# Kernel optimization log

Hardware: AMD Instinct MI355X
Metric: run time of the kernel (lower is better)

The kernel has to match this reference:

```python
import jax, jax.numpy as jnp
import numpy as np

B, S, Dm, H = 2, 2048, 1024, 16
HD = Dm // H            # 64, head dim == rotary dim
INTER = 4096            # intermediate_size (gated: W1 -> 2*INTER)
EPS = 1e-5


def _rotate_half(x):
    x1, x2 = jnp.split(x, 2, axis=-1)
    return jnp.concatenate((-x2, x1), axis=-1)


def _layernorm(x, g, b):
    mu = jnp.mean(x, axis=-1, keepdims=True)
    var = jnp.var(x, axis=-1, keepdims=True)
    return (x - mu) * jax.lax.rsqrt(var + EPS) * g + b


def setup_inputs() -> dict:
    key = jax.random.key(0)
    ks = jax.random.split(key, 12)
    s = 0.02
    hidden_states = jax.random.normal(ks[0], (B, S, Dm), jnp.float32)
    attention_mask = jnp.zeros((B, 1, 1, S), jnp.float32)
    # RoPE angles: pos * inv_freq, shape [S, HD]
    inv_freq = 1.0 / (10000.0 ** (jnp.arange(0, HD, 2, dtype=jnp.float32) / HD))
    ang = jnp.arange(S, dtype=jnp.float32)[:, None] * inv_freq[None, :]
    rope_freqs = jnp.concatenate([ang, ang], axis=-1)  # [S, HD]
    params = {
        'Wq': jax.random.normal(ks[1], (Dm, Dm)) * s, 'bq': jnp.zeros((Dm,)),
        'Wk': jax.random.normal(ks[2], (Dm, Dm)) * s, 'bk': jnp.zeros((Dm,)),
        'Wv': jax.random.normal(ks[3], (Dm, Dm)) * s, 'bv': jnp.zeros((Dm,)),
        'Wo': jax.random.normal(ks[4], (Dm, Dm)) * s, 'bo': jnp.zeros((Dm,)),
        'ln1_g': jnp.ones((Dm,)), 'ln1_b': jnp.zeros((Dm,)),
        'ln2_g': jnp.ones((Dm,)), 'ln2_b': jnp.zeros((Dm,)),
        'W1': jax.random.normal(ks[5], (Dm, 2 * INTER)) * s, 'b1': jnp.zeros((2 * INTER,)),
        'W2': jax.random.normal(ks[6], (INTER, Dm)) * s, 'b2': jnp.zeros((Dm,)),
    }
    return {'hidden_states': hidden_states, 'attention_mask': attention_mask,
            'rope_freqs': rope_freqs, **params}


def reference(hidden_states, attention_mask, rope_freqs,
              Wq, bq, Wk, bk, Wv, bv, Wo, bo,
              ln1_g, ln1_b, ln2_g, ln2_b, W1, b1, W2, b2):
    # ---- attention block (pre-LN) ----
    x = _layernorm(hidden_states, ln1_g, ln1_b)          # [B,S,Dm]
    def heads(t):  # [B,S,Dm] -> [B,H,S,HD]
        return t.reshape(B, S, H, HD).transpose(0, 2, 1, 3)
    q = heads(x @ Wq + bq)
    k = heads(x @ Wk + bk)
    v = heads(x @ Wv + bv)
    # RoPE (full head dim rotated)
    cos = jnp.cos(rope_freqs)[None, None, :, :]          # [1,1,S,HD]
    sin = jnp.sin(rope_freqs)[None, None, :, :]
    q = q * cos + _rotate_half(q) * sin
    k = k * cos + _rotate_half(k) * sin
    scores = jnp.einsum('bhqd,bhkd->bhqk', q, k) / jnp.sqrt(jnp.float32(HD))
    scores = scores + attention_mask
    probs = jax.nn.softmax(scores, axis=-1)
    probs = jnp.where(attention_mask < -1e-5, 0.0, probs)  # masked_fill
    ctx = jnp.einsum('bhqk,bhkd->bhqd', probs, v)
    ctx = ctx.transpose(0, 2, 1, 3).reshape(B, S, Dm)
    hidden = hidden_states + (ctx @ Wo + bo)              # residual
    # ---- MLP block (pre-LN, swiglu) ----
    y = _layernorm(hidden, ln2_g, ln2_b)
    h = y @ W1 + b1
    h0, h1 = jnp.split(h, 2, axis=-1)
    act = h0 * jax.nn.silu(h1)                            # swiglu
    out = hidden + (act @ W2 + b2)
    return out
```

## Files before the change

kernel.cpp:

```cpp
#include <hip/hip_runtime.h>
#include <cstdint>


typedef __bf16 bf16;
typedef __bf16 bf16x8 __attribute__((ext_vector_type(8)));
typedef float f32x4 __attribute__((ext_vector_type(4)));
typedef float f32x16 __attribute__((ext_vector_type(16)));

#define B_ 2
#define S_ 2048
#define DM_ 1024
#define H_ 16
#define HD_ 64
#define INTER_ 4096

#define MFMA16(a, b, c) __builtin_amdgcn_mfma_f32_16x16x32_bf16(a, b, c, 0, 0, 0)
#define MFMA32(a, b, c) __builtin_amdgcn_mfma_f32_32x32x16_bf16(a, b, c, 0, 0, 0)

#if __has_builtin(__builtin_amdgcn_exp2f)
#define EXP2F(x) __builtin_amdgcn_exp2f(x)
#else
#define EXP2F(x) __expf((x) * 0.6931471805599453f)
#endif

__device__ __forceinline__ void cp16(void* lds, const void* g) {
  __builtin_amdgcn_global_load_lds(
      (const __attribute__((address_space(1))) void*)(uintptr_t)g,
      (__attribute__((address_space(3))) void*)(uint32_t)(uintptr_t)lds,
      16, 0, 0);
}

__global__ void transpose4_f32_bf16(const float* __restrict__ w0,
                                    const float* __restrict__ w1,
                                    const float* __restrict__ w2,
                                    const float* __restrict__ w3,
                                    bf16* __restrict__ o0, bf16* __restrict__ o1,
                                    bf16* __restrict__ o2, bf16* __restrict__ o3) {
  __shared__ float tile[32][33];
  const float* in = (blockIdx.z == 0) ? w0 : (blockIdx.z == 1) ? w1
                    : (blockIdx.z == 2) ? w2 : w3;
  bf16* out = (blockIdx.z == 0) ? o0 : (blockIdx.z == 1) ? o1
              : (blockIdx.z == 2) ? o2 : o3;
  int n0 = blockIdx.x * 32, k0 = blockIdx.y * 32;
  int tx = threadIdx.x, ty = threadIdx.y;
#pragma unroll
  for (int i = 0; i < 32; i += 8)
    tile[ty + i][tx] = in[(size_t)(k0 + ty + i) * 1024 + n0 + tx];
  __syncthreads();
#pragma unroll
  for (int i = 0; i < 32; i += 8)
    out[(size_t)(n0 + ty + i) * 1024 + k0 + tx] = (bf16)tile[tx][ty + i];
}

__global__ void transpose_f32_bf16(const float* __restrict__ in,
                                   bf16* __restrict__ out, int K, int N) {
  __shared__ float tile[32][33];
  int n0 = blockIdx.x * 32, k0 = blockIdx.y * 32;
  int tx = threadIdx.x, ty = threadIdx.y;
#pragma unroll
  for (int i = 0; i < 32; i += 8)
    tile[ty + i][tx] = in[(size_t)(k0 + ty + i) * N + n0 + tx];
  __syncthreads();
#pragma unroll
  for (int i = 0; i < 32; i += 8)
    out[(size_t)(n0 + ty + i) * K + k0 + tx] = (bf16)tile[tx][ty + i];
}

__global__ void transpose_w1(const float* __restrict__ in,
                             bf16* __restrict__ out) {
  __shared__ float tile[32][33];
  int n0 = blockIdx.x * 32, k0 = blockIdx.y * 32;
  int tx = threadIdx.x, ty = threadIdx.y;
#pragma unroll
  for (int i = 0; i < 32; i += 8)
    tile[ty + i][tx] = in[(size_t)(k0 + ty + i) * (2 * INTER_) + n0 + tx];
  __syncthreads();
#pragma unroll
  for (int i = 0; i < 32; i += 8) {
    int n = n0 + ty + i;
    int r = ((n & 4095) >> 3) * 16 + ((n >> 12) << 3) + (n & 7);
    out[(size_t)r * DM_ + k0 + tx] = (bf16)tile[tx][ty + i];
  }
}

__global__ void transpose_bf16(const bf16* __restrict__ in,
                               bf16* __restrict__ out, int K, int N) {
  __shared__ bf16 tile[32][33];
  const size_t mo = (size_t)blockIdx.z * K * N;
  int n0 = blockIdx.x * 32, k0 = blockIdx.y * 32;
  int tx = threadIdx.x, ty = threadIdx.y;
#pragma unroll
  for (int i = 0; i < 32; i += 8)
    tile[ty + i][tx] = in[mo + (size_t)(k0 + ty + i) * N + n0 + tx];
  __syncthreads();
#pragma unroll
  for (int i = 0; i < 32; i += 8)
    out[mo + (size_t)(n0 + ty + i) * K + k0 + tx] = tile[tx][ty + i];
}

__global__ __launch_bounds__(256) void ln_bf16(const float* __restrict__ x,
                                               const float* __restrict__ g,
                                               const float* __restrict__ bta,
                                               bf16* __restrict__ out) {
  int row = blockIdx.x;
  int tid = threadIdx.x;
  const float4* xr = (const float4*)(x + (size_t)row * DM_);
  float4 v = xr[tid];
  float s1 = v.x + v.y + v.z + v.w;
  float s2 = v.x * v.x + v.y * v.y + v.z * v.z + v.w * v.w;
#pragma unroll
  for (int off = 32; off; off >>= 1) {
    s1 += __shfl_xor(s1, off);
    s2 += __shfl_xor(s2, off);
  }
  __shared__ float rA[4], rB[4];
  int wave = tid >> 6, lane = tid & 63;
  if (!lane) { rA[wave] = s1; rB[wave] = s2; }
  __syncthreads();
  float t1 = rA[0] + rA[1] + rA[2] + rA[3];
  float t2 = rB[0] + rB[1] + rB[2] + rB[3];
  float mean = t1 * (1.0f / DM_);
  float var = t2 * (1.0f / DM_) - mean * mean;
  float rstd = rsqrtf(var + 1e-5f);
  int col = tid * 4;
  float4 gv = ((const float4*)g)[tid];
  float4 bv = ((const float4*)bta)[tid];
  bf16* o = out + (size_t)row * DM_ + col;
  o[0] = (bf16)((v.x - mean) * rstd * gv.x + bv.x);
  o[1] = (bf16)((v.y - mean) * rstd * gv.y + bv.y);
  o[2] = (bf16)((v.z - mean) * rstd * gv.z + bv.z);
  o[3] = (bf16)((v.w - mean) * rstd * gv.w + bv.w);
}

template <int EPI, int BN>
__global__ __launch_bounds__(256, 2) void gemm_bt(
    const bf16* __restrict__ A, const bf16* __restrict__ Bt,
    const float* __restrict__ b0, const float* __restrict__ b1p,
    const float* __restrict__ b2p, const float* __restrict__ rope,
    const float* __restrict__ resid, void* __restrict__ outp, int N, int K) {
  constexpr int WM = (BN == 128) ? 2 : 1;
  __shared__ __align__(16) bf16 As[128 * 32];
  __shared__ __align__(16) bf16 Bs[BN * 32];
  const int tid = threadIdx.x;
  const int lane = tid & 63, wave = tid >> 6;
  const int col = lane & 31, half = lane >> 5;
  const int mbase = (BN == 128) ? (wave >> 1) * 64 : wave * 32;
  const int nbase = (BN == 128) ? (wave & 1) * 64 : 0;
  const int bm0 = blockIdx.y * 128, bn0 = blockIdx.x * BN;

  f32x16 acc[WM][2];
#pragma unroll
  for (int i = 0; i < WM; ++i)
#pragma unroll
    for (int j = 0; j < 2; ++j)
#pragma unroll
      for (int r = 0; r < 16; ++r) acc[i][j][r] = 0.f;

  for (int k0 = 0; k0 < K; k0 += 32) {
    __syncthreads();
#pragma unroll
    for (int it = 0; it < 2; ++it) {
      int idx = tid + it * 256;
      int row = idx >> 2, chg = (idx & 3) ^ (row & 3);
      cp16(As + (size_t)idx * 8, A + (size_t)(bm0 + row) * K + k0 + chg * 8);
    }
#pragma unroll
    for (int it = 0; it < BN / 64; ++it) {
      int idx = tid + it * 256;
      int row = idx >> 2, chg = (idx & 3) ^ (row & 3);
      cp16(Bs + (size_t)idx * 8, Bt + (size_t)(bn0 + row) * K + k0 + chg * 8);
    }
    __syncthreads();
#pragma unroll
    for (int s = 0; s < 2; ++s) {
      bf16x8 af[WM], bfr[2];
#pragma unroll
      for (int mi = 0; mi < WM; ++mi) {
        int row = mbase + mi * 32 + col;
        af[mi] = *(const bf16x8*)(As + row * 32 + ((s * 2 + half) ^ (row & 3)) * 8);
      }
#pragma unroll
      for (int ni = 0; ni < 2; ++ni) {
        int row = nbase + ni * 32 + col;
        bfr[ni] = *(const bf16x8*)(Bs + row * 32 + ((s * 2 + half) ^ (row & 3)) * 8);
      }
#pragma unroll
      for (int mi = 0; mi < WM; ++mi)
#pragma unroll
        for (int ni = 0; ni < 2; ++ni)
          acc[mi][ni] = MFMA32(af[mi], bfr[ni], acc[mi][ni]);
    }
  }

  if constexpr (EPI == 2) {
    float* o = (float*)outp;
#pragma unroll
    for (int mi = 0; mi < WM; ++mi)
#pragma unroll
      for (int reg = 0; reg < 16; ++reg) {
        int gm = bm0 + mbase + mi * 32 + (reg & 3) + 8 * (reg >> 2) + 4 * half;
        const float* rrow = resid + (size_t)gm * N;
        float* orow = o + (size_t)gm * N;
#pragma unroll
        for (int ni = 0; ni < 2; ++ni) {
          int gn = bn0 + nbase + ni * 32 + col;
          orow[gn] = acc[mi][ni][reg] + b0[gn] + rrow[gn];
        }
      }
  } else if constexpr (EPI == 4) {
    bf16* act = (bf16*)outp;
#pragma unroll
    for (int mi = 0; mi < WM; ++mi)
#pragma unroll
      for (int reg = 0; reg < 16; ++reg) {
        int gm = bm0 + mbase + mi * 32 + (reg & 3) + 8 * (reg >> 2) + 4 * half;
        bf16* arow = act + (size_t)gm * INTER_;
#pragma unroll
        for (int ni = 0; ni < 2; ++ni) {
          int gn = bn0 + nbase + ni * 32 + col;
          int g = gn >> 4, t = gn & 7, hi = (gn >> 3) & 1;
          float val = acc[mi][ni][reg] + b0[g * 8 + t + (hi << 12)];
          float part = __shfl_xor(val, 8);
          if (!hi) {
            float sg = part / (1.0f + __expf(-part));
            arow[g * 8 + t] = (bf16)(val * sg);
          }
        }
      }
  } else {
    bf16* o = (bf16*)outp;
    const int mtx = bn0 >> 10;
    const float* bp = (mtx == 0) ? b0 : (mtx == 1) ? b1p : b2p;
#pragma unroll
    for (int mi = 0; mi < WM; ++mi)
#pragma unroll
      for (int reg = 0; reg < 16; ++reg) {
        int gm = bm0 + mbase + mi * 32 + (reg & 3) + 8 * (reg >> 2) + 4 * half;
        int s = gm & (S_ - 1);
        int bb = gm >> 11;
#pragma unroll
        for (int ni = 0; ni < 2; ++ni) {
          int gn = bn0 + nbase + ni * 32 + col;
          int ci = gn & 1023, hd = gn & 63;
          float val = acc[mi][ni][reg] + bp[ci];
          if (mtx < 2) {
            float part = acc[mi][ni ^ 1][reg] + bp[ci ^ 32];
            if (!(gn & 32)) part = -part;
            float fr = rope[s * HD_ + hd];
            float sn, cs;
            __sincosf(fr, &sn, &cs);
            val = val * cs + part * sn;
            if (mtx == 0) val *= 0.1803368867f;
          }
          o[(size_t)mtx * (32 * S_ * HD_) +
            (((size_t)(bb * H_ + ((gn >> 6) & 15))) * S_ + s) * HD_ + hd] =
              (bf16)val;
        }
      }
  }
}

__global__ __launch_bounds__(512, 2) void flash_attn(
    const bf16* __restrict__ q, const bf16* __restrict__ k,
    const bf16* __restrict__ vt, const float* __restrict__ mask,
    bf16* __restrict__ ctx) {
  __shared__ __align__(16) bf16 Ks[128 * 64];
  __shared__ __align__(16) bf16 Vs[64 * 128];
  __shared__ __align__(16) bf16 Ps[8][16 * 128];

  const int tid = threadIdx.x;
  const int lane = tid & 63, wave = tid >> 6;
  const int c = lane & 15, quad = lane >> 4;
  const int bh = blockIdx.y, b = bh >> 4, h = bh & 15;
  const int q0 = blockIdx.x * 128;

  const bf16* qh = q + (size_t)bh * S_ * HD_;
  const bf16* kh = k + (size_t)bh * S_ * HD_;
  const bf16* vh = vt + (size_t)bh * HD_ * S_;
  const float* mrow = mask + (size_t)b * S_;

  int qrow = q0 + wave * 16 + c;
  bf16x8 qa0 = *(const bf16x8*)(qh + (size_t)qrow * HD_ + quad * 8);
  bf16x8 qa1 = *(const bf16x8*)(qh + (size_t)qrow * HD_ + 32 + quad * 8);

  const f32x4 z4 = {0.f, 0.f, 0.f, 0.f};
  f32x4 o[4] = {z4, z4, z4, z4};
  float l_i[4] = {0.f, 0.f, 0.f, 0.f};

  for (int k0 = 0; k0 < S_; k0 += 128) {
    __syncthreads();
#pragma unroll
    for (int it = 0; it < 2; ++it) {
      int idx = tid + it * 512;
      int row = idx >> 3, chg = (idx & 7) ^ (row & 7);
      cp16(Ks + (size_t)idx * 8, kh + (size_t)(k0 + row) * HD_ + chg * 8);
    }
#pragma unroll
    for (int it = 0; it < 2; ++it) {
      int idx = tid + it * 512;
      int row = idx >> 4, chg = (idx & 15) ^ (row & 15);
      cp16(Vs + (size_t)idx * 8, vh + (size_t)row * S_ + k0 + chg * 8);
    }
    __syncthreads();

    f32x4 sv[8];
    float mv2[8];
#pragma unroll
    for (int tj = 0; tj < 8; ++tj) {
      int krow = tj * 16 + c;
      const bf16* kr = Ks + krow * 64;
      bf16x8 kb0 = *(const bf16x8*)(kr + (quad ^ (krow & 7)) * 8);
      bf16x8 kb1 = *(const bf16x8*)(kr + ((4 + quad) ^ (krow & 7)) * 8);
      sv[tj] = MFMA16(qa0, kb0, z4);
      sv[tj] = MFMA16(qa1, kb1, sv[tj]);
      mv2[tj] = mrow[k0 + krow] * 1.4426950408889634f;
    }

    bf16* pw = Ps[wave];
#pragma unroll
    for (int tj = 0; tj < 8; ++tj) {
      bool msk = mv2[tj] < -1.4426950e-5f;
#pragma unroll
      for (int r = 0; r < 4; ++r) {
        float e = EXP2F(sv[tj][r] + mv2[tj]);
        l_i[r] += e;
        float p = msk ? 0.f : e;
        int prow = quad * 4 + r;
        int chunk = (tj * 2 + (c >> 3)) ^ prow;
        pw[prow * 128 + chunk * 8 + (c & 7)] = (bf16)p;
      }
    }
    asm volatile("s_waitcnt lgkmcnt(0)" ::: "memory");
    bf16x8 pa[4];
#pragma unroll
    for (int ks = 0; ks < 4; ++ks)
      pa[ks] = *(const bf16x8*)(pw + c * 128 + ((ks * 4 + quad) ^ c) * 8);

#pragma unroll
    for (int tn = 0; tn < 4; ++tn) {
      int vrow = tn * 16 + c;
      const bf16* vr = Vs + vrow * 128;
#pragma unroll
      for (int ks = 0; ks < 4; ++ks) {
        bf16x8 vb = *(const bf16x8*)(vr + ((ks * 4 + quad) ^ (vrow & 15)) * 8);
        o[tn] = MFMA16(pa[ks], vb, o[tn]);
      }
    }
  }

#pragma unroll
  for (int r = 0; r < 4; ++r) {
    float l = l_i[r];
#pragma unroll
    for (int off = 1; off < 16; off <<= 1) l += __shfl_xor(l, off);
    float inv = 1.0f / l;
    int qout = q0 + wave * 16 + quad * 4 + r;
    bf16* crow = ctx + ((size_t)(b * S_ + qout)) * DM_ + h * HD_;
#pragma unroll
    for (int tn = 0; tn < 4; ++tn) crow[tn * 16 + c] = (bf16)(o[tn][r] * inv);
  }
}

extern "C" void kernel_launch(void* const* d_in, const int* in_sizes, int n_in,
                              void* d_out, int out_size, void* d_ws,
                              size_t ws_size, hipStream_t stream) {
  const float* hs   = (const float*)d_in[0];
  const float* mask = (const float*)d_in[1];
  const float* rope = (const float*)d_in[2];
  const float* Wq = (const float*)d_in[3];  const float* bq = (const float*)d_in[4];
  const float* Wk = (const float*)d_in[5];  const float* bk = (const float*)d_in[6];
  const float* Wv = (const float*)d_in[7];  const float* bv = (const float*)d_in[8];
  const float* Wo = (const float*)d_in[9];  const float* bo = (const float*)d_in[10];
  const float* g1 = (const float*)d_in[11]; const float* be1 = (const float*)d_in[12];
  const float* g2 = (const float*)d_in[13]; const float* be2 = (const float*)d_in[14];
  const float* W1 = (const float*)d_in[15]; const float* b1 = (const float*)d_in[16];
  const float* W2 = (const float*)d_in[17]; const float* b2 = (const float*)d_in[18];
  float* out = (float*)d_out;
  char* ws = (char*)d_ws;
  const size_t MB = 1ull << 20;

  bf16* Wqkvt = (bf16*)(ws + 0 * MB);
  bf16* Wot = (bf16*)(ws + 6 * MB);
  bf16* W1t = (bf16*)(ws + 8 * MB);
  bf16* W2t = (bf16*)(ws + 24 * MB);
  bf16* xln = (bf16*)(ws + 32 * MB);
  float* hid = (float*)(ws + 40 * MB);
  bf16* qkv = (bf16*)(ws + 56 * MB);
  bf16* vtr = (bf16*)(ws + 80 * MB);
  bf16* ctx = (bf16*)(ws + 88 * MB);
  bf16* act = (bf16*)(ws + 96 * MB);

  dim3 blk(256);
  dim3 tb(32, 8);

  transpose4_f32_bf16<<<dim3(32, 32, 4), tb, 0, stream>>>(
      Wq, Wk, Wv, Wo, Wqkvt, Wqkvt + (1 << 20), Wqkvt + (2 << 20), Wot);
  transpose_w1<<<dim3(256, 32), tb, 0, stream>>>(W1, W1t);
  transpose_f32_bf16<<<dim3(32, 128), tb, 0, stream>>>(W2, W2t, 4096, 1024);

  ln_bf16<<<4096, blk, 0, stream>>>(hs, g1, be1, xln);

  gemm_bt<0, 128><<<dim3(24, 32), blk, 0, stream>>>(
      xln, Wqkvt, bq, bk, bv, rope, nullptr, qkv, 3072, 1024);

  transpose_bf16<<<dim3(2, 64, 32), tb, 0, stream>>>(
      qkv + (size_t)2 * 32 * S_ * HD_, vtr, 2048, 64);

  flash_attn<<<dim3(16, 32), dim3(512), 0, stream>>>(
      qkv, qkv + (size_t)32 * S_ * HD_, vtr, mask, ctx);

  gemm_bt<2, 64><<<dim3(16, 32), blk, 0, stream>>>(
      ctx, Wot, bo, nullptr, nullptr, nullptr, hs, hid, 1024, 1024);

  ln_bf16<<<4096, blk, 0, stream>>>(hid, g2, be2, xln);

  gemm_bt<4, 128><<<dim3(64, 32), blk, 0, stream>>>(
      xln, W1t, b1, nullptr, nullptr, nullptr, nullptr, act, 8192, 1024);

  gemm_bt<2, 64><<<dim3(16, 32), blk, 0, stream>>>(
      act, W2t, b2, nullptr, nullptr, nullptr, hid, out, 1024, 4096);

  (void)in_sizes; (void)n_in; (void)out_size; (void)ws_size;
}
```

Baseline: 518.6 us.

## Switch GEMM to 16x16x32 MFMA tiles with BK=64 K-step

Rewrites the shared GEMM kernel to use 16x16x32 bf16 MFMA fragments instead of 32x32x16, and doubles the K tile from 32 to 64 with a matching 8-way XOR swizzle in LDS. Fewer K iterations halve the number of barriers and global-to-LDS load rounds, and the epilogue mappings (rope pairing, swiglu shuffle, residual) are remapped to the new fragment layout. LDS use doubles, which may affect occupancy, and the smaller MFMA shape needs more LDS fragment reads per FLOP.

```diff
diff --git a/kernel.cpp b/kernel.cpp
--- a/kernel.cpp
+++ b/kernel.cpp
@@ -5,7 +5,6 @@
 typedef __bf16 bf16;
 typedef __bf16 bf16x8 __attribute__((ext_vector_type(8)));
 typedef float f32x4 __attribute__((ext_vector_type(4)));
-typedef float f32x16 __attribute__((ext_vector_type(16)));
 
 #define B_ 2
 #define S_ 2048
@@ -15,7 +14,6 @@
 #define INTER_ 4096
 
 #define MFMA16(a, b, c) __builtin_amdgcn_mfma_f32_16x16x32_bf16(a, b, c, 0, 0, 0)
-#define MFMA32(a, b, c) __builtin_amdgcn_mfma_f32_32x32x16_bf16(a, b, c, 0, 0, 0)
 
 #if __has_builtin(__builtin_amdgcn_exp2f)
 #define EXP2F(x) __builtin_amdgcn_exp2f(x)
@@ -138,88 +136,88 @@
     const float* __restrict__ b0, const float* __restrict__ b1p,
     const float* __restrict__ b2p, const float* __restrict__ rope,
     const float* __restrict__ resid, void* __restrict__ outp, int N, int K) {
-  constexpr int WM = (BN == 128) ? 2 : 1;
-  __shared__ __align__(16) bf16 As[128 * 32];
-  __shared__ __align__(16) bf16 Bs[BN * 32];
+  constexpr int TM = (BN == 128) ? 4 : 2;
+  __shared__ __align__(16) bf16 As[128 * 64];
+  __shared__ __align__(16) bf16 Bs[BN * 64];
   const int tid = threadIdx.x;
   const int lane = tid & 63, wave = tid >> 6;
-  const int col = lane & 31, half = lane >> 5;
-  const int mbase = (BN == 128) ? (wave >> 1) * 64 : wave * 32;
-  const int nbase = (BN == 128) ? (wave & 1) * 64 : 0;
+  const int c = lane & 15, quad = lane >> 4;
+  const int wr = (BN == 128) ? (wave >> 1) : wave;
+  const int wc = (BN == 128) ? (wave & 1) : 0;
+  const int mbase = wr * (16 * TM), nbase = wc * 64;
   const int bm0 = blockIdx.y * 128, bn0 = blockIdx.x * BN;
 
-  f32x16 acc[WM][2];
-#pragma unroll
-  for (int i = 0; i < WM; ++i)
-#pragma unroll
-    for (int j = 0; j < 2; ++j)
-#pragma unroll
-      for (int r = 0; r < 16; ++r) acc[i][j][r] = 0.f;
-
-  for (int k0 = 0; k0 < K; k0 += 32) {
+  f32x4 acc[TM][4];
+  const f32x4 z4 = {0.f, 0.f, 0.f, 0.f};
+#pragma unroll
+  for (int i = 0; i < TM; ++i)
+#pragma unroll
+    for (int j = 0; j < 4; ++j) acc[i][j] = z4;
+
+  for (int k0 = 0; k0 < K; k0 += 64) {
     __syncthreads();
 #pragma unroll
-    for (int it = 0; it < 2; ++it) {
+    for (int it = 0; it < 4; ++it) {
       int idx = tid + it * 256;
-      int row = idx >> 2, chg = (idx & 3) ^ (row & 3);
-      cp16(As + (size_t)idx * 8, A + (size_t)(bm0 + row) * K + k0 + chg * 8);
-    }
-#pragma unroll
-    for (int it = 0; it < BN / 64; ++it) {
+      int row = idx >> 3, g = (idx ^ row) & 7;
+      cp16(As + (size_t)idx * 8, A + (size_t)(bm0 + row) * K + k0 + g * 8);
+    }
+#pragma unroll
+    for (int it = 0; it < BN / 32; ++it) {
       int idx = tid + it * 256;
-      int row = idx >> 2, chg = (idx & 3) ^ (row & 3);
-      cp16(Bs + (size_t)idx * 8, Bt + (size_t)(bn0 + row) * K + k0 + chg * 8);
+      int row = idx >> 3, g = (idx ^ row) & 7;
+      cp16(Bs + (size_t)idx * 8, Bt + (size_t)(bn0 + row) * K + k0 + g * 8);
     }
     __syncthreads();
 #pragma unroll
     for (int s = 0; s < 2; ++s) {
-      bf16x8 af[WM], bfr[2];
-#pragma unroll
-      for (int mi = 0; mi < WM; ++mi) {
-        int row = mbase + mi * 32 + col;
-        af[mi] = *(const bf16x8*)(As + row * 32 + ((s * 2 + half) ^ (row & 3)) * 8);
-      }
-#pragma unroll
-      for (int ni = 0; ni < 2; ++ni) {
-        int row = nbase + ni * 32 + col;
-        bfr[ni] = *(const bf16x8*)(Bs + row * 32 + ((s * 2 + half) ^ (row & 3)) * 8);
-      }
-#pragma unroll
-      for (int mi = 0; mi < WM; ++mi)
-#pragma unroll
-        for (int ni = 0; ni < 2; ++ni)
-          acc[mi][ni] = MFMA32(af[mi], bfr[ni], acc[mi][ni]);
+      bf16x8 af[TM], bfr[4];
+#pragma unroll
+      for (int ti = 0; ti < TM; ++ti) {
+        int row = mbase + ti * 16 + c;
+        af[ti] = *(const bf16x8*)(As + row * 64 + ((s * 4 + quad) ^ (row & 7)) * 8);
+      }
+#pragma unroll
+      for (int tj = 0; tj < 4; ++tj) {
+        int row = nbase + tj * 16 + c;
+        bfr[tj] = *(const bf16x8*)(Bs + row * 64 + ((s * 4 + quad) ^ (row & 7)) * 8);
+      }
+#pragma unroll
+      for (int ti = 0; ti < TM; ++ti)
+#pragma unroll
+        for (int tj = 0; tj < 4; ++tj)
+          acc[ti][tj] = MFMA16(af[ti], bfr[tj], acc[ti][tj]);
     }
   }
 
   if constexpr (EPI == 2) {
     float* o = (float*)outp;
 #pragma unroll
-    for (int mi = 0; mi < WM; ++mi)
-#pragma unroll
-      for (int reg = 0; reg < 16; ++reg) {
-        int gm = bm0 + mbase + mi * 32 + (reg & 3) + 8 * (reg >> 2) + 4 * half;
+    for (int ti = 0; ti < TM; ++ti)
+#pragma unroll
+      for (int r = 0; r < 4; ++r) {
+        int gm = bm0 + mbase + ti * 16 + quad * 4 + r;
         const float* rrow = resid + (size_t)gm * N;
         float* orow = o + (size_t)gm * N;
 #pragma unroll
-        for (int ni = 0; ni < 2; ++ni) {
-          int gn = bn0 + nbase + ni * 32 + col;
-          orow[gn] = acc[mi][ni][reg] + b0[gn] + rrow[gn];
+        for (int tj = 0; tj < 4; ++tj) {
+          int gn = bn0 + nbase + tj * 16 + c;
+          orow[gn] = acc[ti][tj][r] + b0[gn] + rrow[gn];
         }
       }
   } else if constexpr (EPI == 4) {
     bf16* act = (bf16*)outp;
 #pragma unroll
-    for (int mi = 0; mi < WM; ++mi)
-#pragma unroll
-      for (int reg = 0; reg < 16; ++reg) {
-        int gm = bm0 + mbase + mi * 32 + (reg & 3) + 8 * (reg >> 2) + 4 * half;
+    for (int ti = 0; ti < TM; ++ti)
+#pragma unroll
+      for (int r = 0; r < 4; ++r) {
+        int gm = bm0 + mbase + ti * 16 + quad * 4 + r;
         bf16* arow = act + (size_t)gm * INTER_;
 #pragma unroll
-        for (int ni = 0; ni < 2; ++ni) {
-          int gn = bn0 + nbase + ni * 32 + col;
+        for (int tj = 0; tj < 4; ++tj) {
+          int gn = bn0 + nbase + tj * 16 + c;
           int g = gn >> 4, t = gn & 7, hi = (gn >> 3) & 1;
-          float val = acc[mi][ni][reg] + b0[g * 8 + t + (hi << 12)];
+          float val = acc[ti][tj][r] + b0[g * 8 + t + (hi << 12)];
           float part = __shfl_xor(val, 8);
           if (!hi) {
             float sg = part / (1.0f + __expf(-part));
@@ -232,20 +230,22 @@
     const int mtx = bn0 >> 10;
     const float* bp = (mtx == 0) ? b0 : (mtx == 1) ? b1p : b2p;
 #pragma unroll
-    for (int mi = 0; mi < WM; ++mi)
-#pragma unroll
-      for (int reg = 0; reg < 16; ++reg) {
-        int gm = bm0 + mbase + mi * 32 + (reg & 3) + 8 * (reg >> 2) + 4 * half;
+    for (int ti = 0; ti < TM; ++ti)
+#pragma unroll
+      for (int r = 0; r < 4; ++r) {
+        int gm = bm0 + mbase + ti * 16 + quad * 4 + r;
         int s = gm & (S_ - 1);
         int bb = gm >> 11;
 #pragma unroll
-        for (int ni = 0; ni < 2; ++ni) {
-          int gn = bn0 + nbase + ni * 32 + col;
+        for (int tj = 0; tj < 4; ++tj) {
+          int gn = bn0 + nbase + tj * 16 + c;
           int ci = gn & 1023, hd = gn & 63;
-          float val = acc[mi][ni][reg] + bp[ci];
+          float val = acc[ti][tj][r] + bp[ci];
           if (mtx < 2) {
-            float part = acc[mi][ni ^ 1][reg] + bp[ci ^ 32];
-            if (!(gn & 32)) part = -part;
+            int pj = (tj & 2) ? tj - 2 : tj + 2;
+            int ci2 = (tj & 2) ? ci - 32 : ci + 32;
+            float part = acc[ti][pj][r] + bp[ci2];
+            if (!(tj & 2)) part = -part;
             float fr = rope[s * HD_ + hd];
             float sn, cs;
             __sincosf(fr, &sn, &cs);
```

Result: faster. 455.8 us (-12.1%).
